# Optimization experiments

Hardware: AMD Instinct MI355X
Metric: run time of the kernel (lower is better)

The kernel has to match this reference:

```python
import jax, jax.numpy as jnp
import numpy as np

B, N, D, C, K = 32, 4096, 768, 10, 16


def setup_inputs() -> dict:
    key = jax.random.key(0)
    k1, k2, k3, k4, k5 = jax.random.split(key, 5)
    H = jax.random.normal(k1, (B, N, D), dtype=jnp.float32)
    # nn.Linear default init scale ~ 1/sqrt(fan_in)
    sc = 1.0 / np.sqrt(D)
    w_score = jax.random.uniform(k2, (D,), jnp.float32, -sc, sc)
    b_score = jax.random.uniform(k3, (), jnp.float32, -sc, sc)
    W_cls = jax.random.uniform(k4, (D, C), jnp.float32, -sc, sc)
    b_cls = jax.random.uniform(k5, (C,), jnp.float32, -sc, sc)
    return {"H": H, "w_score": w_score, "b_score": b_score,
            "W_cls": W_cls, "b_cls": b_cls}


def reference(H, w_score, b_score, W_cls, b_cls):
    # scores per instance: [B, N]
    s = jnp.einsum("bnd,d->bn", H, w_score) + b_score
    k = min(K, H.shape[1])
    _, topk = jax.lax.top_k(s, k)                      # [B, k] int32
    # gather top-k instances: [B, k, D]
    Hk = jnp.take_along_axis(H, topk[:, :, None], axis=1)
    M = jnp.mean(Hk, axis=1)                           # [B, D]
    # dropout is identity in eval mode
    logits = M @ W_cls + b_cls                         # [B, C]
    # attention mask: scatter 1.0 at topk indices, normalize
    A = jnp.zeros_like(s).at[jnp.arange(H.shape[0])[:, None], topk].set(1.0)
    A = A / jnp.maximum(A.sum(axis=1, keepdims=True), 1e-6)
    return logits, A[:, :, None]
```

## Files before the change

kernel.cpp:

```cpp
#include <hip/hip_runtime.h>
#include <math.h>

#define BB 32
#define NN 4096
#define DD 768
#define CC 10
#define KK 16

__global__ __launch_bounds__(256) void score_kernel(
    const float* __restrict__ H, const float* __restrict__ w,
    const float* __restrict__ b_score, float* __restrict__ s) {
  const int wave_id = blockIdx.x * 4 + (threadIdx.x >> 6);
  const int lane = threadIdx.x & 63;

  const float4* __restrict__ w4 = (const float4*)w;
  const float4 w0 = w4[lane];
  const float4 w1 = w4[lane + 64];
  const float4 w2 = w4[lane + 128];
  const float bs = b_score[0];

  const long row0 = (long)wave_id * 16;
  const float4* __restrict__ H4 = (const float4*)H;

  for (int it = 0; it < 4; ++it) {
    const long r = row0 + it * 4;
    const float4* __restrict__ p = H4 + r * 192;

    float4 h[4][3];
#pragma unroll
    for (int rr = 0; rr < 4; ++rr)
#pragma unroll
      for (int j = 0; j < 3; ++j)
        h[rr][j] = p[rr * 192 + lane + j * 64];

    float acc[4];
#pragma unroll
    for (int rr = 0; rr < 4; ++rr) {
      float a = h[rr][0].x * w0.x + h[rr][0].y * w0.y +
                h[rr][0].z * w0.z + h[rr][0].w * w0.w;
      a += h[rr][1].x * w1.x + h[rr][1].y * w1.y +
           h[rr][1].z * w1.z + h[rr][1].w * w1.w;
      a += h[rr][2].x * w2.x + h[rr][2].y * w2.y +
           h[rr][2].z * w2.z + h[rr][2].w * w2.w;
      acc[rr] = a;
    }

#pragma unroll
    for (int off = 32; off >= 1; off >>= 1) {
#pragma unroll
      for (int rr = 0; rr < 4; ++rr)
        acc[rr] += __shfl_xor(acc[rr], off, 64);
    }

    if (lane == 0) {
      float4 o = {acc[0] + bs, acc[1] + bs, acc[2] + bs, acc[3] + bs};
      ((float4*)s)[r >> 2] = o;
    }
  }
}

__global__ __launch_bounds__(256) void tail_kernel(
    const float* __restrict__ s, const float* __restrict__ H,
    const float* __restrict__ Wc, const float* __restrict__ bc,
    float* __restrict__ logits, float* __restrict__ A) {
  const int b = blockIdx.x;
  const int t = threadIdx.x;
  const int wave = t >> 6;
  const int lane = t & 63;

  __shared__ float wv[4];
  __shared__ int wi[4];
  __shared__ int winners[KK];
  __shared__ float wp[4][CC];

  float v[16];
  {
    const float4* sv4 = (const float4*)(s + (long)b * NN);
    float4 a0 = sv4[t * 4 + 0];
    float4 a1 = sv4[t * 4 + 1];
    float4 a2 = sv4[t * 4 + 2];
    float4 a3 = sv4[t * 4 + 3];
    v[0] = a0.x;  v[1] = a0.y;  v[2] = a0.z;  v[3] = a0.w;
    v[4] = a1.x;  v[5] = a1.y;  v[6] = a1.z;  v[7] = a1.w;
    v[8] = a2.x;  v[9] = a2.y;  v[10] = a2.z; v[11] = a2.w;
    v[12] = a3.x; v[13] = a3.y; v[14] = a3.z; v[15] = a3.w;
  }

  float lv = v[0];
  int li = t * 16;
#pragma unroll
  for (int j = 1; j < 16; ++j)
    if (v[j] > lv) { lv = v[j]; li = t * 16 + j; }

  for (int k = 0; k < KK; ++k) {
    float rv = lv;
    int ri = li;
#pragma unroll
    for (int off = 1; off < 64; off <<= 1) {
      float ov = __shfl_xor(rv, off, 64);
      int oi = __shfl_xor(ri, off, 64);
      if (ov > rv || (ov == rv && oi < ri)) { rv = ov; ri = oi; }
    }
    if (lane == 0) { wv[wave] = rv; wi[wave] = ri; }
    __syncthreads();

    float bv = wv[0];
    int bi = wi[0];
#pragma unroll
    for (int wq = 1; wq < 4; ++wq) {
      float ov = wv[wq];
      int oi = wi[wq];
      if (ov > bv || (ov == bv && oi < bi)) { bv = ov; bi = oi; }
    }
    if (t == 0) winners[k] = bi;

    if ((bi >> 4) == t) {
      const int slot = bi & 15;
#pragma unroll
      for (int j = 0; j < 16; ++j)
        if (j == slot) v[j] = -INFINITY;
      lv = -INFINITY;
      li = t * 16;
#pragma unroll
      for (int j = 0; j < 16; ++j)
        if (v[j] > lv) { lv = v[j]; li = t * 16 + j; }
    }
    __syncthreads();
  }

#pragma unroll
  for (int jj = 0; jj < 4; ++jj) {
    const int q = t + jj * 256;
    const int n0 = q * 4;
    float4 av = {0.f, 0.f, 0.f, 0.f};
#pragma unroll
    for (int k = 0; k < KK; ++k) {
      int d = winners[k] - n0;
      if (d == 0) av.x = 0.0625f;
      else if (d == 1) av.y = 0.0625f;
      else if (d == 2) av.z = 0.0625f;
      else if (d == 3) av.w = 0.0625f;
    }
    ((float4*)(A + (long)b * NN))[q] = av;
  }

  float part[CC];
#pragma unroll
  for (int c = 0; c < CC; ++c) part[c] = 0.f;
  for (int d = t; d < DD; d += 256) {
    float g = 0.f;
#pragma unroll
    for (int k = 0; k < KK; ++k)
      g += H[((long)b * NN + winners[k]) * DD + d];
    g *= (1.f / 16.f);
#pragma unroll
    for (int c = 0; c < CC; ++c) part[c] += g * Wc[d * CC + c];
  }
#pragma unroll
  for (int off = 32; off >= 1; off >>= 1) {
#pragma unroll
    for (int c = 0; c < CC; ++c) part[c] += __shfl_xor(part[c], off, 64);
  }
  if (lane == 0) {
#pragma unroll
    for (int c = 0; c < CC; ++c) wp[wave][c] = part[c];
  }
  __syncthreads();
  if (t < CC) {
    float r = wp[0][t] + wp[1][t] + wp[2][t] + wp[3][t];
    logits[b * CC + t] = r + bc[t];
  }
}

extern "C" void kernel_launch(void* const* d_in, const int* in_sizes, int n_in,
                              void* d_out, int out_size, void* d_ws, size_t ws_size,
                              hipStream_t stream) {
  const float* H = (const float*)d_in[0];
  const float* w_score = (const float*)d_in[1];
  const float* b_score = (const float*)d_in[2];
  const float* W_cls = (const float*)d_in[3];
  const float* b_cls = (const float*)d_in[4];

  float* out = (float*)d_out;
  float* logits = out;
  float* A = out + BB * CC;

  float* s = (float*)d_ws;

  score_kernel<<<2048, 256, 0, stream>>>(H, w_score, b_score, s);
  tail_kernel<<<BB, 256, 0, stream>>>(s, H, W_cls, b_cls, logits, A);
}
```

Before: 105.5 us.

## Fuse score and tail kernels with per-batch atomic counters for overlap

Merges the scoring and top-k/tail kernels into one launch. The first 32 blocks act as consumers that spin on per-batch completion counters, while 1024 producer blocks each score two row ranges and signal per-batch completion with release atomics. This removes the second kernel launch and lets each batch's top-k and gather start as soon as its scores are ready, overlapping with scoring of later batches. It adds a memset launch and spin-waiting blocks that hold CUs. Correctness depends on the producer blocks being scheduled while consumer blocks spin.

```diff
diff --git a/kernel.cpp b/kernel.cpp
--- a/kernel.cpp
+++ b/kernel.cpp
@@ -7,71 +7,90 @@
 #define CC 10
 #define KK 16
 
-__global__ __launch_bounds__(256) void score_kernel(
+#define TAIL_BLOCKS 32
+#define SCORE_BLOCKS 1024
+#define BLOCKS_PER_BATCH 64
+
+__global__ __launch_bounds__(256) void fused_kernel(
     const float* __restrict__ H, const float* __restrict__ w,
-    const float* __restrict__ b_score, float* __restrict__ s) {
-  const int wave_id = blockIdx.x * 4 + (threadIdx.x >> 6);
-  const int lane = threadIdx.x & 63;
-
-  const float4* __restrict__ w4 = (const float4*)w;
-  const float4 w0 = w4[lane];
-  const float4 w1 = w4[lane + 64];
-  const float4 w2 = w4[lane + 128];
-  const float bs = b_score[0];
-
-  const long row0 = (long)wave_id * 16;
-  const float4* __restrict__ H4 = (const float4*)H;
-
-  for (int it = 0; it < 4; ++it) {
-    const long r = row0 + it * 4;
-    const float4* __restrict__ p = H4 + r * 192;
-
-    float4 h[4][3];
-#pragma unroll
-    for (int rr = 0; rr < 4; ++rr)
-#pragma unroll
-      for (int j = 0; j < 3; ++j)
-        h[rr][j] = p[rr * 192 + lane + j * 64];
-
-    float acc[4];
-#pragma unroll
-    for (int rr = 0; rr < 4; ++rr) {
-      float a = h[rr][0].x * w0.x + h[rr][0].y * w0.y +
-                h[rr][0].z * w0.z + h[rr][0].w * w0.w;
-      a += h[rr][1].x * w1.x + h[rr][1].y * w1.y +
-           h[rr][1].z * w1.z + h[rr][1].w * w1.w;
-      a += h[rr][2].x * w2.x + h[rr][2].y * w2.y +
-           h[rr][2].z * w2.z + h[rr][2].w * w2.w;
-      acc[rr] = a;
-    }
-
-#pragma unroll
-    for (int off = 32; off >= 1; off >>= 1) {
-#pragma unroll
-      for (int rr = 0; rr < 4; ++rr)
-        acc[rr] += __shfl_xor(acc[rr], off, 64);
-    }
-
-    if (lane == 0) {
-      float4 o = {acc[0] + bs, acc[1] + bs, acc[2] + bs, acc[3] + bs};
-      ((float4*)s)[r >> 2] = o;
-    }
-  }
-}
-
-__global__ __launch_bounds__(256) void tail_kernel(
-    const float* __restrict__ s, const float* __restrict__ H,
-    const float* __restrict__ Wc, const float* __restrict__ bc,
-    float* __restrict__ logits, float* __restrict__ A) {
-  const int b = blockIdx.x;
+    const float* __restrict__ b_score, const float* __restrict__ Wc,
+    const float* __restrict__ bc, float* __restrict__ s,
+    int* __restrict__ cnt, float* __restrict__ logits,
+    float* __restrict__ A) {
   const int t = threadIdx.x;
   const int wave = t >> 6;
   const int lane = t & 63;
+
+  if (blockIdx.x >= TAIL_BLOCKS) {
+    const int g = blockIdx.x - TAIL_BLOCKS;
+    const float4* __restrict__ w4 = (const float4*)w;
+    const float4 w0 = w4[lane];
+    const float4 w1 = w4[lane + 64];
+    const float4 w2 = w4[lane + 128];
+    const float bs = b_score[0];
+    const float4* __restrict__ H4 = (const float4*)H;
+
+    for (int p = 0; p < 2; ++p) {
+      const long base = (long)p * 65536 + (long)g * 64 + wave * 16;
+      for (int it = 0; it < 4; ++it) {
+        const long r = base + it * 4;
+        const float4* __restrict__ rp = H4 + r * 192;
+
+        float4 h[4][3];
+#pragma unroll
+        for (int rr = 0; rr < 4; ++rr)
+#pragma unroll
+          for (int j = 0; j < 3; ++j)
+            h[rr][j] = rp[rr * 192 + lane + j * 64];
+
+        float acc[4];
+#pragma unroll
+        for (int rr = 0; rr < 4; ++rr) {
+          float a = h[rr][0].x * w0.x + h[rr][0].y * w0.y +
+                    h[rr][0].z * w0.z + h[rr][0].w * w0.w;
+          a += h[rr][1].x * w1.x + h[rr][1].y * w1.y +
+               h[rr][1].z * w1.z + h[rr][1].w * w1.w;
+          a += h[rr][2].x * w2.x + h[rr][2].y * w2.y +
+               h[rr][2].z * w2.z + h[rr][2].w * w2.w;
+          acc[rr] = a;
+        }
+
+#pragma unroll
+        for (int off = 32; off >= 1; off >>= 1) {
+#pragma unroll
+          for (int rr = 0; rr < 4; ++rr)
+            acc[rr] += __shfl_xor(acc[rr], off, 64);
+        }
+
+        if (lane == 0) {
+          float4 o = {acc[0] + bs, acc[1] + bs, acc[2] + bs, acc[3] + bs};
+          ((float4*)s)[r >> 2] = o;
+        }
+      }
+      __syncthreads();
+      if (t == 0) {
+        __threadfence();
+        __hip_atomic_fetch_add(&cnt[p * 16 + (g >> 6)], 1,
+                               __ATOMIC_RELEASE, __HIP_MEMORY_SCOPE_AGENT);
+      }
+    }
+    return;
+  }
+
+  const int b = blockIdx.x;
 
   __shared__ float wv[4];
   __shared__ int wi[4];
   __shared__ int winners[KK];
   __shared__ float wp[4][CC];
+
+  if (t == 0) {
+    while (__hip_atomic_load(&cnt[b], __ATOMIC_ACQUIRE,
+                             __HIP_MEMORY_SCOPE_AGENT) < BLOCKS_PER_BATCH)
+      __builtin_amdgcn_s_sleep(8);
+    __threadfence();
+  }
+  __syncthreads();
 
   float v[16];
   {
@@ -148,13 +167,13 @@
 #pragma unroll
   for (int c = 0; c < CC; ++c) part[c] = 0.f;
   for (int d = t; d < DD; d += 256) {
-    float g = 0.f;
+    float g2 = 0.f;
 #pragma unroll
     for (int k = 0; k < KK; ++k)
-      g += H[((long)b * NN + winners[k]) * DD + d];
-    g *= (1.f / 16.f);
-#pragma unroll
-    for (int c = 0; c < CC; ++c) part[c] += g * Wc[d * CC + c];
+      g2 += H[((long)b * NN + winners[k]) * DD + d];
+    g2 *= (1.f / 16.f);
+#pragma unroll
+    for (int c = 0; c < CC; ++c) part[c] += g2 * Wc[d * CC + c];
   }
 #pragma unroll
   for (int off = 32; off >= 1; off >>= 1) {
@@ -186,7 +205,9 @@
   float* A = out + BB * CC;
 
   float* s = (float*)d_ws;
-
-  score_kernel<<<2048, 256, 0, stream>>>(H, w_score, b_score, s);
-  tail_kernel<<<BB, 256, 0, stream>>>(s, H, W_cls, b_cls, logits, A);
+  int* cnt = (int*)((char*)d_ws + (size_t)BB * NN * sizeof(float));
+
+  hipMemsetAsync(cnt, 0, BB * sizeof(int), stream);
+  fused_kernel<<<TAIL_BLOCKS + SCORE_BLOCKS, 256, 0, stream>>>(
+      H, w_score, b_score, W_cls, b_cls, s, cnt, logits, A);
 }
```

Result: slower. 287.8 us (+172.8%).
